# Kernel tuning notes

Hardware: AMD Instinct MI355X
Metric: run time of the kernel (lower is better)

Reference implementation:

```python
import jax, jax.numpy as jnp
import numpy as np

B, T_NEW, CACHED_MAX = 8, 128, 2048
D_MODEL, N_HEADS = 1024, 16
D_HEAD = D_MODEL // N_HEADS
MAX_TOTAL = CACHED_MAX + T_NEW


def rotate_half(x):
    x1, x2 = x[..., : x.shape[-1] // 2], x[..., x.shape[-1] // 2 :]
    return jnp.concatenate([-x2, x1], axis=-1)


def setup_inputs() -> dict:
    key = jax.random.key(0)
    ks = jax.random.split(key, 16)
    w_scale = D_MODEL ** -0.5  # xavier-ish
    inp = {
        "x_new": jax.random.normal(ks[0], (B, T_NEW, D_MODEL), jnp.float32),
        "past_k": jax.random.normal(ks[1], (B, N_HEADS, CACHED_MAX, D_HEAD), jnp.float32),
        "past_v": jax.random.normal(ks[2], (B, N_HEADS, CACHED_MAX, D_HEAD), jnp.float32),
        "Wq": jax.random.normal(ks[3], (D_MODEL, D_MODEL), jnp.float32) * w_scale,
        "bq": jnp.zeros((D_MODEL,), jnp.float32),
        "Wk": jax.random.normal(ks[4], (D_MODEL, D_MODEL), jnp.float32) * w_scale,
        "bk": jnp.zeros((D_MODEL,), jnp.float32),
        "Wv": jax.random.normal(ks[5], (D_MODEL, D_MODEL), jnp.float32) * w_scale,
        "bv": jnp.zeros((D_MODEL,), jnp.float32),
        "Wo": jax.random.normal(ks[6], (D_MODEL, D_MODEL), jnp.float32) * w_scale,
        "bo": jnp.zeros((D_MODEL,), jnp.float32),
        "inv_freq": 1.0 / (10000.0 ** (jnp.arange(0, D_HEAD, 2, dtype=jnp.float32) / D_HEAD)),
        # ragged lengths; >=1 so every row attends to something
        "past_lengths": jax.random.randint(ks[7], (B,), 1, CACHED_MAX + 1),
        "new_lengths": jax.random.randint(ks[8], (B,), 1, T_NEW + 1),
    }
    return inp


def _attention_fwd(x_new, past_k, past_v, Wq, bq, Wk, bk, Wv, bv, Wo, bo, inv_freq,
                   past_lengths, new_lengths):
    steps = jnp.arange(T_NEW)
    valid_new = steps[None, :] < new_lengths[:, None]            # [B, T_new]

    def proj(W, b):  # torch Linear: x @ W.T + b -> [B, H, T_new, D_head]
        y = jnp.einsum("btm,nm->btn", x_new, W) + b
        return y.reshape(B, T_NEW, N_HEADS, D_HEAD).transpose(0, 2, 1, 3)

    q, k_new, v_new = proj(Wq, bq), proj(Wk, bk), proj(Wv, bv)

    # RoPE at absolute positions past_len + step (0 where invalid)
    positions = jnp.where(valid_new, past_lengths[:, None] + steps[None, :], 0)
    freqs = positions[..., None].astype(jnp.float32) * inv_freq  # [B, T_new, D_head/2]
    emb = jnp.concatenate([freqs, freqs], axis=-1)               # [B, T_new, D_head]
    cos = jnp.cos(emb)[:, None]                                  # [B, 1, T_new, D_head]
    sin = jnp.sin(emb)[:, None]
    q = q * cos + rotate_half(q) * sin
    k_new = k_new * cos + rotate_half(k_new) * sin

    vm = valid_new[:, None, :, None].astype(q.dtype)
    q, k_new, v_new = q * vm, k_new * vm, v_new * vm

    total_lengths = past_lengths + new_lengths
    j = jnp.arange(MAX_TOTAL)
    in_past = (j[None, :] < past_lengths[:, None])[:, None, :, None]       # [B,1,MT,1]
    in_new = ((j[None, :] >= past_lengths[:, None]) &
              (j[None, :] < total_lengths[:, None]))[:, None, :, None]
    idx_new = jnp.clip(j[None, :] - past_lengths[:, None], 0, T_NEW - 1)   # [B, MT]

    past_k_pad = jnp.pad(past_k, ((0, 0), (0, 0), (0, T_NEW), (0, 0)))
    past_v_pad = jnp.pad(past_v, ((0, 0), (0, 0), (0, T_NEW), (0, 0)))
    gather = jax.vmap(lambda xb, ib: xb[:, ib])  # [H,T_new,D], [MT] -> [H,MT,D]
    k_total = jnp.where(in_past, past_k_pad, jnp.where(in_new, gather(k_new, idx_new), 0.0))
    v_total = jnp.where(in_past, past_v_pad, jnp.where(in_new, gather(v_new, idx_new), 0.0))

    attend = j[None, :] < total_lengths[:, None]                  # [B, MT]
    scores = jnp.einsum("bhqd,bhkd->bhqk", q, k_total) * (D_HEAD ** -0.5)
    neg = jnp.asarray(jnp.finfo(scores.dtype).min, scores.dtype)
    scores = jnp.where(attend[:, None, None, :], scores, neg)
    attn = jax.nn.softmax(scores, axis=-1)
    ctx = jnp.einsum("bhqk,bhkd->bhqd", attn, v_total)            # [B,H,T_new,D]

    out = ctx.transpose(0, 2, 1, 3).reshape(B, T_NEW, D_MODEL)
    out = jnp.einsum("btm,nm->btn", out, Wo) + bo
    return out * valid_new[..., None].astype(out.dtype)


def reference(x_new, past_k, past_v, Wq, bq, Wk, bk, Wv, bv, Wo, bo, inv_freq,
              past_lengths, new_lengths):
    return _attention_fwd(x_new, past_k, past_v, Wq, bq, Wk, bk, Wv, bv, Wo, bo,
                          inv_freq, past_lengths, new_lengths)
```

## Files before the change

### kernel.cpp

```cpp
#include <hip/hip_runtime.h>

#define NB 8
#define TNEW 128
#define CMAX 2048
#define DMODEL 1024
#define NH 16
#define DH 64

typedef float f32x4 __attribute__((ext_vector_type(4)));
typedef short short8 __attribute__((ext_vector_type(8)));
typedef short short4v __attribute__((ext_vector_type(4)));

__device__ __forceinline__ short f2bf(float x) {
  unsigned u = __float_as_uint(x);
  u += 0x7FFFu + ((u >> 16) & 1u);
  return (short)(u >> 16);
}
__device__ __forceinline__ float bf2f(short s) {
  return __uint_as_float(((unsigned)(unsigned short)s) << 16);
}
__device__ __forceinline__ short8 cvt8(f32x4 a, f32x4 b) {
  short8 o;
  o[0] = f2bf(a.x); o[1] = f2bf(a.y); o[2] = f2bf(a.z); o[3] = f2bf(a.w);
  o[4] = f2bf(b.x); o[5] = f2bf(b.y); o[6] = f2bf(b.z); o[7] = f2bf(b.w);
  return o;
}

__global__ __launch_bounds__(256) void cvt5_bf16(
    const float* __restrict__ s0, const float* __restrict__ s1,
    const float* __restrict__ s2, const float* __restrict__ s3,
    const float* __restrict__ s4, short* __restrict__ dst) {
  const int seg = blockIdx.x >> 10;
  const int i = (blockIdx.x & 1023) * 256 + threadIdx.x;
  const float* src = seg == 0 ? s0 : seg == 1 ? s1 : seg == 2 ? s2 : seg == 3 ? s3 : s4;
  f32x4 v = *(const f32x4*)(src + (size_t)i * 4);
  short4v o;
  o.x = f2bf(v.x); o.y = f2bf(v.y); o.z = f2bf(v.z); o.w = f2bf(v.w);
  *(short4v*)(dst + (size_t)seg * (1u << 20) + (size_t)i * 4) = o;
}

template<int MODE>
__global__ __launch_bounds__(256) void gemm64(
    const short* __restrict__ A, const short* __restrict__ Wbase,
    void* __restrict__ Out, const float* __restrict__ bias0,
    const float* __restrict__ bias1, const float* __restrict__ bias2,
    const int* __restrict__ new_len)
{
  constexpr int LDT = 40;
  __shared__ short As[64 * LDT];
  __shared__ short Bs[64 * LDT];
  const int n0 = blockIdx.x * 64, m0 = blockIdx.y * 64, z = blockIdx.z;
  const short* Wp = Wbase + (size_t)z * (DMODEL * DMODEL);
  const float* bias = (MODE == 0) ? (z == 0 ? bias0 : (z == 1 ? bias1 : bias2)) : bias0;
  const int tid = threadIdx.x, lane = tid & 63, w = tid >> 6;
  const int wm = (w >> 1) * 32, wn = (w & 1) * 32;
  const int lr = lane & 15, lk = lane >> 4;

  const int srow = tid >> 2, soff = (tid & 3) * 8;
  const short* Ag = A  + (size_t)(m0 + srow) * DMODEL + soff;
  const short* Bg = Wp + (size_t)(n0 + srow) * DMODEL + soff;
  short* Al = As + srow * LDT + soff;
  short* Bl = Bs + srow * LDT + soff;

  short8 va = *(const short8*)(Ag);
  short8 vb = *(const short8*)(Bg);
  f32x4 acc[2][2] = {};
  for (int kt = 0; kt < DMODEL / 32; ++kt) {
    __syncthreads();
    *(short8*)Al = va;
    *(short8*)Bl = vb;
    if (kt < DMODEL / 32 - 1) {
      va = *(const short8*)(Ag + (kt + 1) * 32);
      vb = *(const short8*)(Bg + (kt + 1) * 32);
    }
    __syncthreads();
    short8 af[2], bfr[2];
    af[0]  = *(const short8*)(As + (wm + lr) * LDT + lk * 8);
    af[1]  = *(const short8*)(As + (wm + 16 + lr) * LDT + lk * 8);
    bfr[0] = *(const short8*)(Bs + (wn + lr) * LDT + lk * 8);
    bfr[1] = *(const short8*)(Bs + (wn + 16 + lr) * LDT + lk * 8);
#pragma unroll
    for (int i = 0; i < 2; ++i)
#pragma unroll
      for (int j = 0; j < 2; ++j)
        acc[i][j] = __builtin_amdgcn_mfma_f32_16x16x32_bf16(af[i], bfr[j], acc[i][j], 0, 0, 0);
  }
#pragma unroll
  for (int i = 0; i < 2; ++i) {
#pragma unroll
    for (int j = 0; j < 2; ++j) {
      const int col = n0 + wn + j * 16 + lr;
      const float bcol = bias[col];
#pragma unroll
      for (int r = 0; r < 4; ++r) {
        const int row = m0 + wm + i * 16 + lk * 4 + r;
        float v = acc[i][j][r] + bcol;
        if (MODE == 0) {
          ((short*)Out)[(size_t)z * (NB * TNEW * DMODEL) + (size_t)row * DMODEL + col] = f2bf(v);
        } else {
          const int bb = row >> 7, t = row & 127;
          ((float*)Out)[(size_t)row * DMODEL + col] = (t < new_len[bb]) ? v : 0.0f;
        }
      }
    }
  }
}

__global__ __launch_bounds__(256) void rope_mask(
    short* __restrict__ qb, short* __restrict__ kb, short* __restrict__ vb,
    const float* __restrict__ inv_freq, const int* __restrict__ past_len,
    const int* __restrict__ new_len)
{
  const int idx = blockIdx.x * 256 + threadIdx.x;
  const int d = idx & 31;
  const int h = (idx >> 5) & 15;
  const int t = (idx >> 9) & 127;
  const int b = idx >> 16;
  const bool valid = t < new_len[b];
  const float pos = (float)(past_len[b] + t);
  float sn, cs;
  sincosf(pos * inv_freq[d], &sn, &cs);
  const size_t base = (size_t)(b * 128 + t) * DMODEL + h * 64 + d;
  const float q1 = bf2f(qb[base]), q2 = bf2f(qb[base + 32]);
  const float k1 = bf2f(kb[base]), k2 = bf2f(kb[base + 32]);
  qb[base]      = valid ? f2bf(q1 * cs - q2 * sn) : (short)0;
  qb[base + 32] = valid ? f2bf(q2 * cs + q1 * sn) : (short)0;
  kb[base]      = valid ? f2bf(k1 * cs - k2 * sn) : (short)0;
  kb[base + 32] = valid ? f2bf(k2 * cs + k1 * sn) : (short)0;
  if (!valid) { vb[base] = 0; vb[base + 32] = 0; }
}

__global__ __launch_bounds__(512) void attn_split(
    const float* __restrict__ pk, const float* __restrict__ pv,
    const short* __restrict__ qb, const short* __restrict__ kb,
    const short* __restrict__ vb, float* __restrict__ Opart,
    float* __restrict__ Ml, const int* __restrict__ past_len,
    const int* __restrict__ new_len, int splits)
{
  constexpr int LDT = 72;
  __shared__ short Kl[64 * LDT];
  __shared__ short Vt[64 * LDT];
  __shared__ short Pl[128 * LDT];
  const int bh = blockIdx.x, b = bh >> 4, h = bh & 15;
  const int s = blockIdx.y;
  const int past = past_len[b];
  const int total = past + new_len[b];
  const int tid = threadIdx.x, lane = tid & 63, w = tid >> 6;
  const int lr = lane & 15, lk = lane >> 4;

  const int nt = (total + 63) >> 6;

  float* mlp = Ml + (size_t)(bh * splits + s) * 256;
  float* op  = Opart + (size_t)(bh * splits + s) * (128 * 64);

  if (s >= nt) {
#pragma unroll
    for (int r = 0; r < 4; ++r) {
      const int q = w * 16 + lk * 4 + r;
      if (lr == 0) { mlp[q] = -3.0e38f; mlp[128 + q] = 0.f; }
    }
    return;
  }

  short8 qf0, qf1;
  {
    const short* qrow = qb + (size_t)(b * 128 + w * 16 + lr) * DMODEL + h * 64;
    qf0 = *(const short8*)(qrow + lk * 8);
    qf1 = *(const short8*)(qrow + 32 + lk * 8);
  }
  float m_run[4], l_run[4];
  f32x4 acc[4] = {};
#pragma unroll
  for (int r = 0; r < 4; ++r) { m_run[r] = -3.0e38f; l_run[r] = 0.f; }

  const int jr = tid >> 3, seg = tid & 7;

  f32x4 kA = {}, kB = {}, vA = {}, vB = {};
  short8 kN = {}, vN = {};
  int smode = 2;
  auto stage_issue = [&](int t) {
    const int j = t * 64 + jr;
    if (j < past) {
      smode = 0;
      const float* kp = pk + ((size_t)(b * 16 + h) * CMAX + j) * 64 + seg * 8;
      const float* vp = pv + ((size_t)(b * 16 + h) * CMAX + j) * 64 + seg * 8;
      kA = *(const f32x4*)kp; kB = *(const f32x4*)(kp + 4);
      vA = *(const f32x4*)vp; vB = *(const f32x4*)(vp + 4);
    } else if (j < total) {
      smode = 1;
      const short* kp = kb + (size_t)(b * 128 + (j - past)) * DMODEL + h * 64 + seg * 8;
      const short* vp = vb + (size_t)(b * 128 + (j - past)) * DMODEL + h * 64 + seg * 8;
      kN = *(const short8*)kp;
      vN = *(const short8*)vp;
    } else {
      smode = 2;
    }
  };

  stage_issue(s);
  for (int kt = s; kt < nt; kt += splits) {
    __syncthreads();
    {
      short8 kr = {}, vr = {};
      if (smode == 0) { kr = cvt8(kA, kB); vr = cvt8(vA, vB); }
      else if (smode == 1) { kr = kN; vr = vN; }
      *(short8*)(Kl + jr * LDT + seg * 8) = kr;
#pragma unroll
      for (int i = 0; i < 8; ++i) Vt[(seg * 8 + i) * LDT + (jr ^ (seg * 8))] = vr[i];
    }
    if (kt + splits < nt) stage_issue(kt + splits);
    __syncthreads();

    f32x4 sc[4];
    __builtin_amdgcn_s_setprio(1);
#pragma unroll
    for (int nf = 0; nf < 4; ++nf) {
      short8 k0 = *(const short8*)(Kl + (nf * 16 + lr) * LDT + lk * 8);
      short8 k1 = *(const short8*)(Kl + (nf * 16 + lr) * LDT + 32 + lk * 8);
      f32x4 zv = {};
      zv = __builtin_amdgcn_mfma_f32_16x16x32_bf16(qf0, k0, zv, 0, 0, 0);
      sc[nf] = __builtin_amdgcn_mfma_f32_16x16x32_bf16(qf1, k1, zv, 0, 0, 0);
    }
    __builtin_amdgcn_s_setprio(0);
    const int kg0 = kt * 64;
    float pmax[4] = {-3.0e38f, -3.0e38f, -3.0e38f, -3.0e38f};
#pragma unroll
    for (int nf = 0; nf < 4; ++nf) {
      const bool ok = (kg0 + nf * 16 + lr) < total;
#pragma unroll
      for (int r = 0; r < 4; ++r) {
        const float sv = ok ? sc[nf][r] * 0.125f : -3.0e38f;
        sc[nf][r] = sv;
        pmax[r] = fmaxf(pmax[r], sv);
      }
    }
#pragma unroll
    for (int r = 0; r < 4; ++r) {
#pragma unroll
      for (int off = 1; off < 16; off <<= 1)
        pmax[r] = fmaxf(pmax[r], __shfl_xor(pmax[r], off));
    }
    float alpha[4], rsum[4];
#pragma unroll
    for (int r = 0; r < 4; ++r) {
      const float mn = fmaxf(m_run[r], pmax[r]);
      alpha[r] = __expf(m_run[r] - mn);
      m_run[r] = mn;
      rsum[r] = 0.f;
    }
#pragma unroll
    for (int nf = 0; nf < 4; ++nf)
#pragma unroll
      for (int r = 0; r < 4; ++r) {
        const float p = __expf(sc[nf][r] - m_run[r]);
        sc[nf][r] = p;
        rsum[r] += p;
      }
#pragma unroll
    for (int r = 0; r < 4; ++r) {
#pragma unroll
      for (int off = 1; off < 16; off <<= 1)
        rsum[r] += __shfl_xor(rsum[r], off);
      l_run[r] = l_run[r] * alpha[r] + rsum[r];
    }
#pragma unroll
    for (int nf = 0; nf < 4; ++nf)
#pragma unroll
      for (int r = 0; r < 4; ++r) acc[nf][r] *= alpha[r];

#pragma unroll
    for (int nf = 0; nf < 4; ++nf)
#pragma unroll
      for (int r = 0; r < 4; ++r)
        Pl[(w * 16 + lk * 4 + r) * LDT + nf * 16 + lr] = f2bf(sc[nf][r]);
    __builtin_amdgcn_s_setprio(1);
#pragma unroll
    for (int kf = 0; kf < 2; ++kf) {
      short8 pf = *(const short8*)(Pl + (w * 16 + lr) * LDT + kf * 32 + lk * 8);
#pragma unroll
      for (int nf = 0; nf < 4; ++nf) {
        const int dd = nf * 16 + lr;
        short8 vf = *(const short8*)(Vt + dd * LDT + ((kf * 32 + lk * 8) ^ (dd & 56)));
        acc[nf] = __builtin_amdgcn_mfma_f32_16x16x32_bf16(pf, vf, acc[nf], 0, 0, 0);
      }
    }
    __builtin_amdgcn_s_setprio(0);
  }
#pragma unroll
  for (int nf = 0; nf < 4; ++nf)
#pragma unroll
    for (int r = 0; r < 4; ++r) {
      const int q = w * 16 + lk * 4 + r, d = nf * 16 + lr;
      op[(size_t)q * 64 + d] = acc[nf][r];
    }
#pragma unroll
  for (int r = 0; r < 4; ++r) {
    const int q = w * 16 + lk * 4 + r;
    if (lr == 0) { mlp[q] = m_run[r]; mlp[128 + q] = l_run[r]; }
  }
}

__global__ __launch_bounds__(256) void attn_combine(
    const float* __restrict__ Opart, const float* __restrict__ Ml,
    short* __restrict__ ctxb, int splits)
{
  const int bh = blockIdx.x, b = bh >> 4, h = bh & 15;
  const int q = blockIdx.y * 16 + (threadIdx.x >> 4);
  const int dv = (threadIdx.x & 15) * 4;
  const float* mlb = Ml + (size_t)bh * splits * 256;
  float mstar = -3.0e38f;
  for (int s = 0; s < splits; ++s)
    mstar = fmaxf(mstar, mlb[s * 256 + q]);
  float lsum = 0.f;
  f32x4 o = {};
  for (int s = 0; s < splits; ++s) {
    const float ws = __expf(mlb[s * 256 + q] - mstar);
    lsum += ws * mlb[s * 256 + 128 + q];
    f32x4 ov = *(const f32x4*)(Opart + ((size_t)(bh * splits + s) * 128 + q) * 64 + dv);
    o.x += ws * ov.x; o.y += ws * ov.y; o.z += ws * ov.z; o.w += ws * ov.w;
  }
  const float inv = 1.0f / lsum;
  short4v r;
  r.x = f2bf(o.x * inv); r.y = f2bf(o.y * inv); r.z = f2bf(o.z * inv); r.w = f2bf(o.w * inv);
  *(short4v*)(ctxb + (size_t)(b * 128 + q) * DMODEL + h * 64 + dv) = r;
}

extern "C" void kernel_launch(void* const* d_in, const int* in_sizes, int n_in,
                              void* d_out, int out_size, void* d_ws, size_t ws_size,
                              hipStream_t stream) {
  const float* x      = (const float*)d_in[0];
  const float* past_k = (const float*)d_in[1];
  const float* past_v = (const float*)d_in[2];
  const float* Wq = (const float*)d_in[3];
  const float* bq = (const float*)d_in[4];
  const float* Wk = (const float*)d_in[5];
  const float* bk = (const float*)d_in[6];
  const float* Wv = (const float*)d_in[7];
  const float* bv = (const float*)d_in[8];
  const float* Wo = (const float*)d_in[9];
  const float* bo = (const float*)d_in[10];
  const float* inv_freq = (const float*)d_in[11];
  const int* past_len = (const int*)d_in[12];
  const int* new_len  = (const int*)d_in[13];

  short* wsb = (short*)d_ws;
  const size_t M1 = 1u << 20;
  short* Xb  = wsb;
  short* Wqb = wsb + 1 * M1;
  short* Wob = wsb + 4 * M1;
  short* qb  = wsb + 5 * M1;
  short* kb  = wsb + 6 * M1;
  short* vb  = wsb + 7 * M1;
  short* ctx = wsb + 8 * M1;
  float* Opart = (float*)(wsb + 9 * M1);

  int splits = 1;
  for (int s = 8; s >= 1; s >>= 1) {
    size_t need = 9 * M1 * sizeof(short) +
                  (size_t)s * 128 * (128 * 64 + 256) * sizeof(float);
    if (need <= ws_size) { splits = s; break; }
  }
  float* Ml = Opart + (size_t)128 * splits * (128 * 64);

  cvt5_bf16<<<5120, 256, 0, stream>>>(x, Wq, Wk, Wv, Wo, wsb);

  gemm64<0><<<dim3(16, 16, 3), 256, 0, stream>>>(Xb, Wqb, (void*)qb, bq, bk, bv, nullptr);
  rope_mask<<<2048, 256, 0, stream>>>(qb, kb, vb, inv_freq, past_len, new_len);
  attn_split<<<dim3(128, splits), 512, 0, stream>>>(past_k, past_v, qb, kb, vb,
                                                    Opart, Ml, past_len, new_len, splits);
  attn_combine<<<dim3(128, 8), 256, 0, stream>>>(Opart, Ml, ctx, splits);
  gemm64<1><<<dim3(16, 16, 1), 256, 0, stream>>>(ctx, Wob, d_out, bo, nullptr, nullptr, new_len);
}
```

Baseline: 76.34 us.

## Fuse RoPE into QKV GEMM epilogue, skip invalid rows, restructure attention pipeline

Removes the separate rope_mask kernel by applying rotary embedding in the QKV GEMM epilogue, with each warp remapped to hold paired columns d and d+32. The GEMM loop is double-buffered in registers with explicit lgkm waits and barriers, and QKV tiles whose rows are all beyond new_len are skipped. The attention kernel uses branchless staging, packed bf16 conversion instructions and a flattened grid, and warps whose query rows are invalid skip compute. The combine kernel also skips invalid queries and zero-weight splits. The risk is that skipped Q/K/V rows are left uninitialized instead of zeroed; this relies on masking downstream (K/V beyond total and invalid outputs are already masked).

```diff
diff --git a/kernel.cpp b/kernel.cpp
--- a/kernel.cpp
+++ b/kernel.cpp
@@ -10,6 +10,7 @@
 typedef float f32x4 __attribute__((ext_vector_type(4)));
 typedef short short8 __attribute__((ext_vector_type(8)));
 typedef short short4v __attribute__((ext_vector_type(4)));
+typedef unsigned uint4v __attribute__((ext_vector_type(4)));
 
 __device__ __forceinline__ short f2bf(float x) {
   unsigned u = __float_as_uint(x);
@@ -20,11 +21,22 @@
   return __uint_as_float(((unsigned)(unsigned short)s) << 16);
 }
 __device__ __forceinline__ short8 cvt8(f32x4 a, f32x4 b) {
-  short8 o;
-  o[0] = f2bf(a.x); o[1] = f2bf(a.y); o[2] = f2bf(a.z); o[3] = f2bf(a.w);
-  o[4] = f2bf(b.x); o[5] = f2bf(b.y); o[6] = f2bf(b.z); o[7] = f2bf(b.w);
-  return o;
-}
+  uint4v t;
+  asm("v_cvt_pk_bf16_f32 %0, %1, %2" : "=v"(t.x) : "v"(a.x), "v"(a.y));
+  asm("v_cvt_pk_bf16_f32 %0, %1, %2" : "=v"(t.y) : "v"(a.z), "v"(a.w));
+  asm("v_cvt_pk_bf16_f32 %0, %1, %2" : "=v"(t.z) : "v"(b.x), "v"(b.y));
+  asm("v_cvt_pk_bf16_f32 %0, %1, %2" : "=v"(t.w) : "v"(b.z), "v"(b.w));
+  return __builtin_bit_cast(short8, t);
+}
+
+#define LGKM0_BAR()                                            \
+  __builtin_amdgcn_sched_barrier(0);                           \
+  asm volatile("s_waitcnt lgkmcnt(0)" ::: "memory");           \
+  __builtin_amdgcn_sched_barrier(0);                           \
+  __builtin_amdgcn_s_barrier()
+#define TAIL_BAR()                                             \
+  __builtin_amdgcn_sched_barrier(0);                           \
+  __builtin_amdgcn_s_barrier()
 
 __global__ __launch_bounds__(256) void cvt5_bf16(
     const float* __restrict__ s0, const float* __restrict__ s1,
@@ -44,16 +56,18 @@
     const short* __restrict__ A, const short* __restrict__ Wbase,
     void* __restrict__ Out, const float* __restrict__ bias0,
     const float* __restrict__ bias1, const float* __restrict__ bias2,
-    const int* __restrict__ new_len)
+    const int* __restrict__ new_len, const float* __restrict__ inv_freq,
+    const int* __restrict__ past_len)
 {
   constexpr int LDT = 40;
   __shared__ short As[64 * LDT];
   __shared__ short Bs[64 * LDT];
   const int n0 = blockIdx.x * 64, m0 = blockIdx.y * 64, z = blockIdx.z;
+  if (MODE == 0 && (m0 & 64) && new_len[m0 >> 7] <= 64) return;
   const short* Wp = Wbase + (size_t)z * (DMODEL * DMODEL);
   const float* bias = (MODE == 0) ? (z == 0 ? bias0 : (z == 1 ? bias1 : bias2)) : bias0;
   const int tid = threadIdx.x, lane = tid & 63, w = tid >> 6;
-  const int wm = (w >> 1) * 32, wn = (w & 1) * 32;
+  const int wm = (w >> 1) * 32, wn2 = (w & 1) * 16;
   const int lr = lane & 15, lk = lane >> 4;
 
   const int srow = tid >> 2, soff = (tid & 3) * 8;
@@ -62,75 +76,83 @@
   short* Al = As + srow * LDT + soff;
   short* Bl = Bs + srow * LDT + soff;
 
-  short8 va = *(const short8*)(Ag);
-  short8 vb = *(const short8*)(Bg);
+  short8 va0 = *(const short8*)(Ag);
+  short8 vb0 = *(const short8*)(Bg);
+  short8 va1, vb1;
   f32x4 acc[2][2] = {};
-  for (int kt = 0; kt < DMODEL / 32; ++kt) {
-    __syncthreads();
-    *(short8*)Al = va;
-    *(short8*)Bl = vb;
-    if (kt < DMODEL / 32 - 1) {
-      va = *(const short8*)(Ag + (kt + 1) * 32);
-      vb = *(const short8*)(Bg + (kt + 1) * 32);
-    }
-    __syncthreads();
-    short8 af[2], bfr[2];
-    af[0]  = *(const short8*)(As + (wm + lr) * LDT + lk * 8);
-    af[1]  = *(const short8*)(As + (wm + 16 + lr) * LDT + lk * 8);
-    bfr[0] = *(const short8*)(Bs + (wn + lr) * LDT + lk * 8);
-    bfr[1] = *(const short8*)(Bs + (wn + 16 + lr) * LDT + lk * 8);
-#pragma unroll
-    for (int i = 0; i < 2; ++i)
-#pragma unroll
-      for (int j = 0; j < 2; ++j)
-        acc[i][j] = __builtin_amdgcn_mfma_f32_16x16x32_bf16(af[i], bfr[j], acc[i][j], 0, 0, 0);
-  }
-#pragma unroll
-  for (int i = 0; i < 2; ++i) {
-#pragma unroll
-    for (int j = 0; j < 2; ++j) {
-      const int col = n0 + wn + j * 16 + lr;
-      const float bcol = bias[col];
+
+#define GEMM_PHASE(CURA, CURB, NXTA, NXTB, KNEXT)                          \
+  {                                                                        \
+    *(short8*)Al = CURA;                                                   \
+    *(short8*)Bl = CURB;                                                   \
+    NXTA = *(const short8*)(Ag + (KNEXT) * 32);                            \
+    NXTB = *(const short8*)(Bg + (KNEXT) * 32);                            \
+    LGKM0_BAR();                                                           \
+    short8 af0 = *(const short8*)(As + (wm + lr) * LDT + lk * 8);          \
+    short8 af1 = *(const short8*)(As + (wm + 16 + lr) * LDT + lk * 8);     \
+    short8 bg0 = *(const short8*)(Bs + (wn2 + lr) * LDT + lk * 8);         \
+    short8 bg1 = *(const short8*)(Bs + (wn2 + 32 + lr) * LDT + lk * 8);    \
+    acc[0][0] = __builtin_amdgcn_mfma_f32_16x16x32_bf16(af0, bg0, acc[0][0], 0, 0, 0); \
+    acc[0][1] = __builtin_amdgcn_mfma_f32_16x16x32_bf16(af0, bg1, acc[0][1], 0, 0, 0); \
+    acc[1][0] = __builtin_amdgcn_mfma_f32_16x16x32_bf16(af1, bg0, acc[1][0], 0, 0, 0); \
+    acc[1][1] = __builtin_amdgcn_mfma_f32_16x16x32_bf16(af1, bg1, acc[1][1], 0, 0, 0); \
+    TAIL_BAR();                                                            \
+  }
+
+  for (int kt = 0; kt < DMODEL / 32; kt += 2) {
+    const int k1 = kt + 1;
+    const int k2 = (kt + 2 < DMODEL / 32) ? kt + 2 : DMODEL / 32 - 1;
+    GEMM_PHASE(va0, vb0, va1, vb1, k1);
+    GEMM_PHASE(va1, vb1, va0, vb0, k2);
+  }
+#undef GEMM_PHASE
+
+  const int colb = n0 + wn2 + lr;
+  const float b0 = bias[colb], b1 = bias[colb + 32];
+
+  if (MODE == 0 && z <= 1) {
+    const int bb = m0 >> 7;
+    const int pbase = past_len[bb];
+    const float fr = inv_freq[(wn2 + lr) & 31];
+    short* outp = (short*)Out + (size_t)z * (NB * TNEW * DMODEL);
+#pragma unroll
+    for (int i = 0; i < 2; ++i) {
 #pragma unroll
       for (int r = 0; r < 4; ++r) {
         const int row = m0 + wm + i * 16 + lk * 4 + r;
-        float v = acc[i][j][r] + bcol;
+        const float pos = (float)(pbase + (row & 127));
+        float sn, cs;
+        sincosf(pos * fr, &sn, &cs);
+        const float a0 = acc[i][0][r] + b0;
+        const float a1 = acc[i][1][r] + b1;
+        outp[(size_t)row * DMODEL + colb]      = f2bf(a0 * cs - a1 * sn);
+        outp[(size_t)row * DMODEL + colb + 32] = f2bf(a1 * cs + a0 * sn);
+      }
+    }
+  } else {
+#pragma unroll
+    for (int i = 0; i < 2; ++i) {
+#pragma unroll
+      for (int r = 0; r < 4; ++r) {
+        const int row = m0 + wm + i * 16 + lk * 4 + r;
+        const float a0 = acc[i][0][r] + b0;
+        const float a1 = acc[i][1][r] + b1;
         if (MODE == 0) {
-          ((short*)Out)[(size_t)z * (NB * TNEW * DMODEL) + (size_t)row * DMODEL + col] = f2bf(v);
+          short* outp = (short*)Out + (size_t)z * (NB * TNEW * DMODEL);
+          outp[(size_t)row * DMODEL + colb]      = f2bf(a0);
+          outp[(size_t)row * DMODEL + colb + 32] = f2bf(a1);
         } else {
           const int bb = row >> 7, t = row & 127;
-          ((float*)Out)[(size_t)row * DMODEL + col] = (t < new_len[bb]) ? v : 0.0f;
+          const bool ok = t < new_len[bb];
+          ((float*)Out)[(size_t)row * DMODEL + colb]      = ok ? a0 : 0.0f;
+          ((float*)Out)[(size_t)row * DMODEL + colb + 32] = ok ? a1 : 0.0f;
         }
       }
     }
   }
 }
 
-__global__ __launch_bounds__(256) void rope_mask(
-    short* __restrict__ qb, short* __restrict__ kb, short* __restrict__ vb,
-    const float* __restrict__ inv_freq, const int* __restrict__ past_len,
-    const int* __restrict__ new_len)
-{
-  const int idx = blockIdx.x * 256 + threadIdx.x;
-  const int d = idx & 31;
-  const int h = (idx >> 5) & 15;
-  const int t = (idx >> 9) & 127;
-  const int b = idx >> 16;
-  const bool valid = t < new_len[b];
-  const float pos = (float)(past_len[b] + t);
-  float sn, cs;
-  sincosf(pos * inv_freq[d], &sn, &cs);
-  const size_t base = (size_t)(b * 128 + t) * DMODEL + h * 64 + d;
-  const float q1 = bf2f(qb[base]), q2 = bf2f(qb[base + 32]);
-  const float k1 = bf2f(kb[base]), k2 = bf2f(kb[base + 32]);
-  qb[base]      = valid ? f2bf(q1 * cs - q2 * sn) : (short)0;
-  qb[base + 32] = valid ? f2bf(q2 * cs + q1 * sn) : (short)0;
-  kb[base]      = valid ? f2bf(k1 * cs - k2 * sn) : (short)0;
-  kb[base + 32] = valid ? f2bf(k2 * cs + k1 * sn) : (short)0;
-  if (!valid) { vb[base] = 0; vb[base + 32] = 0; }
-}
-
-__global__ __launch_bounds__(512) void attn_split(
+__global__ __launch_bounds__(512, 4) void attn_split(
     const float* __restrict__ pk, const float* __restrict__ pv,
     const short* __restrict__ qb, const short* __restrict__ kb,
     const short* __restrict__ vb, float* __restrict__ Opart,
@@ -141,10 +163,12 @@
   __shared__ short Kl[64 * LDT];
   __shared__ short Vt[64 * LDT];
   __shared__ short Pl[128 * LDT];
-  const int bh = blockIdx.x, b = bh >> 4, h = bh & 15;
-  const int s = blockIdx.y;
+  const int id = blockIdx.x;
+  const int bh = id / splits, s = id - bh * splits;
+  const int b = bh >> 4, h = bh & 15;
   const int past = past_len[b];
-  const int total = past + new_len[b];
+  const int nlen = new_len[b];
+  const int total = past + nlen;
   const int tid = threadIdx.x, lane = tid & 63, w = tid >> 6;
   const int lr = lane & 15, lk = lane >> 4;
 
@@ -162,8 +186,9 @@
     return;
   }
 
-  short8 qf0, qf1;
-  {
+  const bool wvalid = (w * 16) < nlen;
+  short8 qf0 = {}, qf1 = {};
+  if (wvalid) {
     const short* qrow = qb + (size_t)(b * 128 + w * 16 + lr) * DMODEL + h * 64;
     qf0 = *(const short8*)(qrow + lk * 8);
     qf1 = *(const short8*)(qrow + 32 + lk * 8);
@@ -174,138 +199,154 @@
   for (int r = 0; r < 4; ++r) { m_run[r] = -3.0e38f; l_run[r] = 0.f; }
 
   const int jr = tid >> 3, seg = tid & 7;
-
-  f32x4 kA = {}, kB = {}, vA = {}, vB = {};
-  short8 kN = {}, vN = {};
-  int smode = 2;
-  auto stage_issue = [&](int t) {
-    const int j = t * 64 + jr;
-    if (j < past) {
-      smode = 0;
-      const float* kp = pk + ((size_t)(b * 16 + h) * CMAX + j) * 64 + seg * 8;
-      const float* vp = pv + ((size_t)(b * 16 + h) * CMAX + j) * 64 + seg * 8;
-      kA = *(const f32x4*)kp; kB = *(const f32x4*)(kp + 4);
-      vA = *(const f32x4*)vp; vB = *(const f32x4*)(vp + 4);
-    } else if (j < total) {
-      smode = 1;
-      const short* kp = kb + (size_t)(b * 128 + (j - past)) * DMODEL + h * 64 + seg * 8;
-      const short* vp = vb + (size_t)(b * 128 + (j - past)) * DMODEL + h * 64 + seg * 8;
-      kN = *(const short8*)kp;
-      vN = *(const short8*)vp;
-    } else {
-      smode = 2;
-    }
-  };
-
-  stage_issue(s);
+  const float* pkb = pk + ((size_t)(b * 16 + h) * CMAX) * 64 + seg * 8;
+  const float* pvb = pv + ((size_t)(b * 16 + h) * CMAX) * 64 + seg * 8;
+  const short* kbb = kb + (size_t)(b * 128) * DMODEL + h * 64 + seg * 8;
+  const short* vbb = vb + (size_t)(b * 128) * DMODEL + h * 64 + seg * 8;
+
+  f32x4 kF0, kF1, vF0, vF1;
+  short8 kN, vN;
+  bool pr0, pr1;
+
+#define STAGE_ISSUE(T)                                                        \
+  {                                                                           \
+    const int j_ = (T) * 64 + jr;                                             \
+    const int jp = min(j_, past - 1);                   \
+    const int jn = min(max(j_ - past, 0), TNEW - 1);                          \
+    pr0 = j_ < past;                                                          \
+    pr1 = j_ < total;                                                         \
+    kF0 = *(const f32x4*)(pkb + (size_t)jp * 64);                             \
+    kF1 = *(const f32x4*)(pkb + (size_t)jp * 64 + 4);                         \
+    vF0 = *(const f32x4*)(pvb + (size_t)jp * 64);                             \
+    vF1 = *(const f32x4*)(pvb + (size_t)jp * 64 + 4);                         \
+    kN  = *(const short8*)(kbb + (size_t)jn * DMODEL);                        \
+    vN  = *(const short8*)(vbb + (size_t)jn * DMODEL);                        \
+  }
+
+  STAGE_ISSUE(s);
   for (int kt = s; kt < nt; kt += splits) {
-    __syncthreads();
     {
-      short8 kr = {}, vr = {};
-      if (smode == 0) { kr = cvt8(kA, kB); vr = cvt8(vA, vB); }
-      else if (smode == 1) { kr = kN; vr = vN; }
+      const short8 z8 = {};
+      short8 kc = cvt8(kF0, kF1);
+      short8 vc = cvt8(vF0, vF1);
+      short8 kr = pr0 ? kc : (pr1 ? kN : z8);
+      short8 vr = pr0 ? vc : (pr1 ? vN : z8);
       *(short8*)(Kl + jr * LDT + seg * 8) = kr;
 #pragma unroll
       for (int i = 0; i < 8; ++i) Vt[(seg * 8 + i) * LDT + (jr ^ (seg * 8))] = vr[i];
     }
-    if (kt + splits < nt) stage_issue(kt + splits);
-    __syncthreads();
-
-    f32x4 sc[4];
-    __builtin_amdgcn_s_setprio(1);
-#pragma unroll
-    for (int nf = 0; nf < 4; ++nf) {
-      short8 k0 = *(const short8*)(Kl + (nf * 16 + lr) * LDT + lk * 8);
-      short8 k1 = *(const short8*)(Kl + (nf * 16 + lr) * LDT + 32 + lk * 8);
-      f32x4 zv = {};
-      zv = __builtin_amdgcn_mfma_f32_16x16x32_bf16(qf0, k0, zv, 0, 0, 0);
-      sc[nf] = __builtin_amdgcn_mfma_f32_16x16x32_bf16(qf1, k1, zv, 0, 0, 0);
-    }
-    __builtin_amdgcn_s_setprio(0);
-    const int kg0 = kt * 64;
-    float pmax[4] = {-3.0e38f, -3.0e38f, -3.0e38f, -3.0e38f};
-#pragma unroll
-    for (int nf = 0; nf < 4; ++nf) {
-      const bool ok = (kg0 + nf * 16 + lr) < total;
-#pragma unroll
-      for (int r = 0; r < 4; ++r) {
-        const float sv = ok ? sc[nf][r] * 0.125f : -3.0e38f;
-        sc[nf][r] = sv;
-        pmax[r] = fmaxf(pmax[r], sv);
-      }
-    }
+    STAGE_ISSUE(kt + splits);
+    LGKM0_BAR();
+
+    if (wvalid) {
+      f32x4 sc[4];
+      __builtin_amdgcn_s_setprio(1);
+#pragma unroll
+      for (int nf = 0; nf < 4; ++nf) {
+        short8 k0 = *(const short8*)(Kl + (nf * 16 + lr) * LDT + lk * 8);
+        short8 k1 = *(const short8*)(Kl + (nf * 16 + lr) * LDT + 32 + lk * 8);
+        f32x4 zv = {};
+        zv = __builtin_amdgcn_mfma_f32_16x16x32_bf16(qf0, k0, zv, 0, 0, 0);
+        sc[nf] = __builtin_amdgcn_mfma_f32_16x16x32_bf16(qf1, k1, zv, 0, 0, 0);
+      }
+      __builtin_amdgcn_s_setprio(0);
+      const int kg0 = kt * 64;
+      float pmax[4] = {-3.0e38f, -3.0e38f, -3.0e38f, -3.0e38f};
+#pragma unroll
+      for (int nf = 0; nf < 4; ++nf) {
+        const bool ok = (kg0 + nf * 16 + lr) < total;
+#pragma unroll
+        for (int r = 0; r < 4; ++r) {
+          const float sv = ok ? sc[nf][r] * 0.125f : -3.0e38f;
+          sc[nf][r] = sv;
+          pmax[r] = fmaxf(pmax[r], sv);
+        }
+      }
+#pragma unroll
+      for (int r = 0; r < 4; ++r) {
+#pragma unroll
+        for (int off = 1; off < 16; off <<= 1)
+          pmax[r] = fmaxf(pmax[r], __shfl_xor(pmax[r], off));
+      }
+      float alpha[4], rsum[4];
+#pragma unroll
+      for (int r = 0; r < 4; ++r) {
+        const float mn = fmaxf(m_run[r], pmax[r]);
+        alpha[r] = __expf(m_run[r] - mn);
+        m_run[r] = mn;
+        rsum[r] = 0.f;
+      }
+#pragma unroll
+      for (int nf = 0; nf < 4; ++nf)
+#pragma unroll
+        for (int r = 0; r < 4; ++r) {
+          const float p = __expf(sc[nf][r] - m_run[r]);
+          sc[nf][r] = p;
+          rsum[r] += p;
+        }
+#pragma unroll
+      for (int r = 0; r < 4; ++r) {
+#pragma unroll
+        for (int off = 1; off < 16; off <<= 1)
+          rsum[r] += __shfl_xor(rsum[r], off);
+        l_run[r] = l_run[r] * alpha[r] + rsum[r];
+      }
+#pragma unroll
+      for (int nf = 0; nf < 4; ++nf)
+#pragma unroll
+        for (int r = 0; r < 4; ++r) acc[nf][r] *= alpha[r];
+
+#pragma unroll
+      for (int nf = 0; nf < 4; ++nf)
+#pragma unroll
+        for (int r = 0; r < 4; ++r)
+          Pl[(w * 16 + lk * 4 + r) * LDT + nf * 16 + lr] = f2bf(sc[nf][r]);
+      __builtin_amdgcn_s_setprio(1);
+#pragma unroll
+      for (int kf = 0; kf < 2; ++kf) {
+        short8 pf = *(const short8*)(Pl + (w * 16 + lr) * LDT + kf * 32 + lk * 8);
+#pragma unroll
+        for (int nf = 0; nf < 4; ++nf) {
+          const int dd = nf * 16 + lr;
+          short8 vf = *(const short8*)(Vt + dd * LDT + ((kf * 32 + lk * 8) ^ (dd & 56)));
+          acc[nf] = __builtin_amdgcn_mfma_f32_16x16x32_bf16(pf, vf, acc[nf], 0, 0, 0);
+        }
+      }
+      __builtin_amdgcn_s_setprio(0);
+    }
+    TAIL_BAR();
+  }
+#undef STAGE_ISSUE
+
+  if (wvalid) {
+#pragma unroll
+    for (int nf = 0; nf < 4; ++nf)
+#pragma unroll
+      for (int r = 0; r < 4; ++r) {
+        const int q = w * 16 + lk * 4 + r, d = nf * 16 + lr;
+        op[(size_t)q * 64 + d] = acc[nf][r];
+      }
 #pragma unroll
     for (int r = 0; r < 4; ++r) {
-#pragma unroll
-      for (int off = 1; off < 16; off <<= 1)
-        pmax[r] = fmaxf(pmax[r], __shfl_xor(pmax[r], off));
-    }
-    float alpha[4], rsum[4];
+      const int q = w * 16 + lk * 4 + r;
+      if (lr == 0) { mlp[q] = m_run[r]; mlp[128 + q] = l_run[r]; }
+    }
+  } else {
 #pragma unroll
     for (int r = 0; r < 4; ++r) {
-      const float mn = fmaxf(m_run[r], pmax[r]);
-      alpha[r] = __expf(m_run[r] - mn);
-      m_run[r] = mn;
-      rsum[r] = 0.f;
-    }
-#pragma unroll
-    for (int nf = 0; nf < 4; ++nf)
-#pragma unroll
-      for (int r = 0; r < 4; ++r) {
-        const float p = __expf(sc[nf][r] - m_run[r]);
-        sc[nf][r] = p;
-        rsum[r] += p;
-      }
-#pragma unroll
-    for (int r = 0; r < 4; ++r) {
-#pragma unroll
-      for (int off = 1; off < 16; off <<= 1)
-        rsum[r] += __shfl_xor(rsum[r], off);
-      l_run[r] = l_run[r] * alpha[r] + rsum[r];
-    }
-#pragma unroll
-    for (int nf = 0; nf < 4; ++nf)
-#pragma unroll
-      for (int r = 0; r < 4; ++r) acc[nf][r] *= alpha[r];
-
-#pragma unroll
-    for (int nf = 0; nf < 4; ++nf)
-#pragma unroll
-      for (int r = 0; r < 4; ++r)
-        Pl[(w * 16 + lk * 4 + r) * LDT + nf * 16 + lr] = f2bf(sc[nf][r]);
-    __builtin_amdgcn_s_setprio(1);
-#pragma unroll
-    for (int kf = 0; kf < 2; ++kf) {
-      short8 pf = *(const short8*)(Pl + (w * 16 + lr) * LDT + kf * 32 + lk * 8);
-#pragma unroll
-      for (int nf = 0; nf < 4; ++nf) {
-        const int dd = nf * 16 + lr;
-        short8 vf = *(const short8*)(Vt + dd * LDT + ((kf * 32 + lk * 8) ^ (dd & 56)));
-        acc[nf] = __builtin_amdgcn_mfma_f32_16x16x32_bf16(pf, vf, acc[nf], 0, 0, 0);
-      }
-    }
-    __builtin_amdgcn_s_setprio(0);
-  }
-#pragma unroll
-  for (int nf = 0; nf < 4; ++nf)
-#pragma unroll
-    for (int r = 0; r < 4; ++r) {
-      const int q = w * 16 + lk * 4 + r, d = nf * 16 + lr;
-      op[(size_t)q * 64 + d] = acc[nf][r];
-    }
-#pragma unroll
-  for (int r = 0; r < 4; ++r) {
-    const int q = w * 16 + lk * 4 + r;
-    if (lr == 0) { mlp[q] = m_run[r]; mlp[128 + q] = l_run[r]; }
+      const int q = w * 16 + lk * 4 + r;
+      if (lr == 0) { mlp[q] = -3.0e38f; mlp[128 + q] = 0.f; }
+    }
   }
 }
 
 __global__ __launch_bounds__(256) void attn_combine(
     const float* __restrict__ Opart, const float* __restrict__ Ml,
-    short* __restrict__ ctxb, int splits)
+    short* __restrict__ ctxb, const int* __restrict__ new_len, int splits)
 {
   const int bh = blockIdx.x, b = bh >> 4, h = bh & 15;
   const int q = blockIdx.y * 16 + (threadIdx.x >> 4);
+  if (q >= new_len[b]) return;
   const int dv = (threadIdx.x & 15) * 4;
   const float* mlb = Ml + (size_t)bh * splits * 256;
   float mstar = -3.0e38f;
@@ -316,8 +357,10 @@
   for (int s = 0; s < splits; ++s) {
     const float ws = __expf(mlb[s * 256 + q] - mstar);
     lsum += ws * mlb[s * 256 + 128 + q];
-    f32x4 ov = *(const f32x4*)(Opart + ((size_t)(bh * splits + s) * 128 + q) * 64 + dv);
-    o.x += ws * ov.x; o.y += ws * ov.y; o.z += ws * ov.z; o.w += ws * ov.w;
+    if (ws > 0.f) {
+      f32x4 ov = *(const f32x4*)(Opart + ((size_t)(bh * splits + s) * 128 + q) * 64 + dv);
+      o.x += ws * ov.x; o.y += ws * ov.y; o.z += ws * ov.z; o.w += ws * ov.w;
+    }
   }
   const float inv = 1.0f / lsum;
   short4v r;
@@ -364,10 +407,11 @@
 
   cvt5_bf16<<<5120, 256, 0, stream>>>(x, Wq, Wk, Wv, Wo, wsb);
 
-  gemm64<0><<<dim3(16, 16, 3), 256, 0, stream>>>(Xb, Wqb, (void*)qb, bq, bk, bv, nullptr);
-  rope_mask<<<2048, 256, 0, stream>>>(qb, kb, vb, inv_freq, past_len, new_len);
-  attn_split<<<dim3(128, splits), 512, 0, stream>>>(past_k, past_v, qb, kb, vb,
-                                                    Opart, Ml, past_len, new_len, splits);
-  attn_combine<<<dim3(128, 8), 256, 0, stream>>>(Opart, Ml, ctx, splits);
-  gemm64<1><<<dim3(16, 16, 1), 256, 0, stream>>>(ctx, Wob, d_out, bo, nullptr, nullptr, new_len);
-}
+  gemm64<0><<<dim3(16, 16, 3), 256, 0, stream>>>(Xb, Wqb, (void*)qb, bq, bk, bv,
+                                                 new_len, inv_freq, past_len);
+  attn_split<<<128 * splits, 512, 0, stream>>>(past_k, past_v, qb, kb, vb,
+                                               Opart, Ml, past_len, new_len, splits);
+  attn_combine<<<dim3(128, 8), 256, 0, stream>>>(Opart, Ml, ctx, new_len, splits);
+  gemm64<1><<<dim3(16, 16, 1), 256, 0, stream>>>(ctx, Wob, d_out, bo, nullptr, nullptr,
+                                                 new_len, nullptr, nullptr);
+}
```

Result: faster. 67.65 us (-11.4%).
